# Kernel optimization log

Measured on AMD Instinct MI355X. Metric: run time of the kernel, lower is better.

Reference implementation:

```python
import jax, jax.numpy as jnp
import numpy as np

DIM = 1024
NUM_HEADS = 16
DIM_HEAD = 64
FEATURE_DIM = 64
INNER = NUM_HEADS * DIM_HEAD
EPS = 1e-6


def setup_inputs() -> dict:
    key = jax.random.key(0)
    ks = jax.random.split(key, 7)
    x = jax.random.normal(ks[0], (4, 8192, DIM), dtype=jnp.float32)
    s = 1.0 / np.sqrt(DIM)
    Wq = jax.random.normal(ks[1], (DIM, INNER), dtype=jnp.float32) * s
    Wk = jax.random.normal(ks[2], (DIM, INNER), dtype=jnp.float32) * s
    Wv = jax.random.normal(ks[3], (DIM, INNER), dtype=jnp.float32) * s
    proj = jax.random.normal(ks[4], (DIM_HEAD, FEATURE_DIM), dtype=jnp.float32) / np.sqrt(FEATURE_DIM)
    Wo = jax.random.normal(ks[5], (INNER, DIM), dtype=jnp.float32) * (1.0 / np.sqrt(INNER))
    bo = jnp.zeros((DIM,), dtype=jnp.float32)
    return {"x": x, "Wq": Wq, "Wk": Wk, "Wv": Wv, "proj": proj, "Wo": Wo, "bo": bo}


def _feature_map(t, proj):
    # t: [b, h, n, d] -> relu(t @ proj) + eps : [b, h, n, f]
    return jax.nn.relu(jnp.einsum('bhnd,df->bhnf', t, proj)) + EPS


def reference(x, Wq, Wk, Wv, proj, Wo, bo):
    b, n, _ = x.shape
    def split_heads(t):
        return t.reshape(b, n, NUM_HEADS, DIM_HEAD).transpose(0, 2, 1, 3)  # [b,h,n,d]
    q = split_heads(x @ Wq)
    k = split_heads(x @ Wk)
    v = split_heads(x @ Wv)
    qf = _feature_map(q, proj)  # [b,h,n,f]
    kf = _feature_map(k, proj)  # [b,h,n,f]
    kv = jnp.einsum('bhnf,bhnd->bhfd', kf, v)          # [b,h,f,d]
    k_sum = kf.sum(axis=-2)                             # [b,h,f]
    num = jnp.einsum('bhnf,bhfd->bhnd', qf, kv)         # [b,h,n,d]
    den = jnp.einsum('bhnf,bhf->bhn', qf, k_sum) + EPS  # [b,h,n]
    out = num / den[..., None]
    out = out.transpose(0, 2, 1, 3).reshape(b, n, INNER)
    return out @ Wo + bo
```

## Files before the change

kernel.cpp:

```cpp
#include <hip/hip_runtime.h>

typedef unsigned short u16;
typedef unsigned int u32;
typedef __attribute__((ext_vector_type(4))) float f32x4;
typedef __attribute__((ext_vector_type(4))) u16 u16x4;
typedef __attribute__((ext_vector_type(8))) u16 u16x8;
typedef __attribute__((ext_vector_type(8))) __bf16 bf16x8;

#define FLA_EPS 1e-6f

__device__ __forceinline__ u16 f2b(float f) {
  union { float f; u32 u; } v; v.f = f;
  u32 r = v.u + 0x7FFFu + ((v.u >> 16) & 1u);
  return (u16)(r >> 16);
}
__device__ __forceinline__ float b2f(u16 h) {
  union { u32 u; float f; } v; v.u = ((u32)h) << 16; return v.f;
}
__device__ __forceinline__ void g2l16(const void* g, void* l) {
  __builtin_amdgcn_global_load_lds((__attribute__((address_space(1))) void*)g,
                                   (__attribute__((address_space(3))) void*)l,
                                   16, 0, 0);
}

__global__ void __launch_bounds__(256) cast_f32_bf16(const float* __restrict__ in,
                                                     u16* __restrict__ out) {
  size_t i = (size_t)blockIdx.x * 256 + threadIdx.x;
  const f32x4* p = (const f32x4*)in + i * 2;
  f32x4 a = p[0], b = p[1];
  u16x8 r;
  r[0] = f2b(a[0]); r[1] = f2b(a[1]); r[2] = f2b(a[2]); r[3] = f2b(a[3]);
  r[4] = f2b(b[0]); r[5] = f2b(b[1]); r[6] = f2b(b[2]); r[7] = f2b(b[3]);
  ((u16x8*)out)[i] = r;
}

__global__ void __launch_bounds__(256) transpose_cast(const float* __restrict__ W,
                                                      u16* __restrict__ Wt, int dim) {
  __shared__ float tile[64][65];
  const int t = threadIdx.x;
  const int k0 = blockIdx.x * 64, n0 = blockIdx.y * 64;
  const int r = t >> 4, c4 = (t & 15) * 4;
#pragma unroll
  for (int i = 0; i < 4; ++i) {
    f32x4 vv = *(const f32x4*)(W + (size_t)(k0 + r + i * 16) * dim + n0 + c4);
    tile[r + i * 16][c4 + 0] = vv[0];
    tile[r + i * 16][c4 + 1] = vv[1];
    tile[r + i * 16][c4 + 2] = vv[2];
    tile[r + i * 16][c4 + 3] = vv[3];
  }
  __syncthreads();
#pragma unroll
  for (int i = 0; i < 4; ++i) {
    int nrow = r + i * 16;
    u16x4 o;
#pragma unroll
    for (int j = 0; j < 4; ++j) o[j] = f2b(tile[c4 + j][nrow]);
    *(u16x4*)(Wt + (size_t)(n0 + nrow) * dim + k0 + c4) = o;
  }
}

__global__ void __launch_bounds__(256) fold_w(const float* __restrict__ Wq,
                                              const float* __restrict__ Wk,
                                              const float* __restrict__ proj,
                                              u16* __restrict__ WqkvT) {
  __shared__ float Wt[64][65];
  __shared__ float P[64][64];
  const int t = threadIdx.x;
  const int kbase = blockIdx.x * 64, h = blockIdx.y, sel = blockIdx.z;
  const float* W = sel ? Wk : Wq;
  {
    int row = t >> 2, cb = (t & 3) * 16;
#pragma unroll
    for (int i = 0; i < 4; ++i) {
      f32x4 vv = *(const f32x4*)(W + (size_t)(kbase + row) * 1024 + h * 64 + cb + i * 4);
      Wt[row][cb + i * 4 + 0] = vv[0]; Wt[row][cb + i * 4 + 1] = vv[1];
      Wt[row][cb + i * 4 + 2] = vv[2]; Wt[row][cb + i * 4 + 3] = vv[3];
      f32x4 pp = *(const f32x4*)(proj + (size_t)row * 64 + cb + i * 4);
      P[row][cb + i * 4 + 0] = pp[0]; P[row][cb + i * 4 + 1] = pp[1];
      P[row][cb + i * 4 + 2] = pp[2]; P[row][cb + i * 4 + 3] = pp[3];
    }
  }
  __syncthreads();
  const int kk = t & 63, fg = (t >> 6) * 16;
  float acc[16] = {};
  for (int d = 0; d < 64; ++d) {
    float w = Wt[kk][d];
#pragma unroll
    for (int ff = 0; ff < 16; ++ff) acc[ff] = fmaf(w, P[d][fg + ff], acc[ff]);
  }
#pragma unroll
  for (int ff = 0; ff < 16; ++ff)
    WqkvT[(size_t)(sel * 1024 + h * 64 + fg + ff) * 1024 + kbase + kk] = f2b(acc[ff]);
}

template <int NB, bool QKV>
__global__ void __launch_bounds__(512, 2) gemm256(const u16* __restrict__ Ax,
                                                  const u16* __restrict__ Bt,
                                                  u16* __restrict__ qo, u16* __restrict__ ko,
                                                  u16* __restrict__ vo,
                                                  float* __restrict__ Cf,
                                                  const float* __restrict__ bias) {
  extern __shared__ __align__(16) u16 lds[];
  const int tid = threadIdx.x;
  const int flat = blockIdx.x;
  const int xcd = flat & 7, slot = flat >> 3;
  const int pos = slot & 7, g = slot >> 3;
  const int nc = g % NB, mc = g / NB;
  const int m0 = (xcd * 16 + mc * 8 + pos) * 256;
  const int n0 = nc * 256;
  const int w = tid >> 6, l = tid & 63, quad = l >> 4, lr = l & 15;
  const int wm = w >> 2, wn = w & 3;
  u16* const A0 = lds;
  u16* const B0 = lds + 16384;
  u16* const A1 = lds + 32768;
  u16* const B1 = lds + 49152;
  const int c0 = ((quad * 16) ^ ((lr & 7) << 4)) >> 1;
  const int c1 = ((64 + quad * 16) ^ ((lr & 7) << 4)) >> 1;
  const int rst = tid >> 3;
  const int ksw8 = ((tid & 7) ^ (rst & 7)) * 8;
  const int tid8 = tid * 8;

  f32x4 acc[8][4] = {};
  bf16x8 af[4][2], bf[4][2];

#define STG(SRC, ROW0, KT, DST) do {                                         \
    const u16* s_ = (SRC) + (size_t)((ROW0) + rst) * 1024 + (KT) + ksw8;     \
    g2l16(s_, (DST) + tid8);                                                 \
    g2l16(s_ + 64 * 1024, (DST) + 4096 + tid8);                              \
  } while (0)

#define LDA_(BASE, MH) do {                                                  \
    const u16* ap_ = (BASE) + wm * 8192;                                     \
    _Pragma("unroll")                                                        \
    for (int ii = 0; ii < 4; ++ii) {                                         \
      const int ro_ = ((MH) * 64 + ii * 16 + lr) * 64;                       \
      af[ii][0] = *(const bf16x8*)(ap_ + ro_ + c0);                          \
      af[ii][1] = *(const bf16x8*)(ap_ + ro_ + c1);                          \
    } } while (0)

#define LDB_(BASE, NH) do {                                                  \
    const u16* bp_ = (BASE) + (wn >> 1) * 8192 + (wn & 1) * 4096;            \
    _Pragma("unroll")                                                        \
    for (int jj = 0; jj < 2; ++jj) {                                         \
      const int ro_ = (((NH) * 2 + jj) * 16 + lr) * 64;                      \
      bf[(NH) * 2 + jj][0] = *(const bf16x8*)(bp_ + ro_ + c0);               \
      bf[(NH) * 2 + jj][1] = *(const bf16x8*)(bp_ + ro_ + c1);               \
    } } while (0)

#define MFMA16(MH, NH)                                                       \
    _Pragma("unroll")                                                        \
    for (int ii = 0; ii < 4; ++ii)                                           \
      _Pragma("unroll")                                                      \
      for (int jj = 0; jj < 2; ++jj)                                         \
        _Pragma("unroll")                                                    \
        for (int ks = 0; ks < 2; ++ks)                                       \
          acc[(MH) * 4 + ii][(NH) * 2 + jj] =                                \
              __builtin_amdgcn_mfma_f32_16x16x32_bf16(                       \
                  af[ii][ks], bf[(NH) * 2 + jj][ks],                         \
                  acc[(MH) * 4 + ii][(NH) * 2 + jj], 0, 0, 0);

#define BARMFMA(MH, NH) do {                                                 \
    __builtin_amdgcn_s_barrier();                                            \
    asm volatile("s_waitcnt lgkmcnt(0)" ::: "memory");                       \
    __builtin_amdgcn_sched_barrier(0);                                       \
    __builtin_amdgcn_s_setprio(1);                                           \
    MFMA16(MH, NH);                                                          \
    __builtin_amdgcn_s_setprio(0);                                           \
    __builtin_amdgcn_s_barrier();                                            \
  } while (0)

  STG(Ax, m0, 0, A0);  STG(Ax, m0 + 128, 0, A0 + 8192);
  STG(Bt, n0, 0, B0);  STG(Bt, n0 + 128, 0, B0 + 8192);
  STG(Bt, n0, 64, B1); STG(Bt, n0 + 128, 64, B1 + 8192);
  asm volatile("s_waitcnt vmcnt(4)" ::: "memory");
  __builtin_amdgcn_s_barrier();

  for (int it = 0; it < 8; ++it) {
    const bool lastI = (it == 7);
    const int ko = it * 128;
    LDA_(A0, 0); LDB_(B0, 0);
    STG(Ax, m0, ko + 64, A1);
    BARMFMA(0, 0);
    LDB_(B0, 1);
    STG(Ax, m0 + 128, ko + 64, A1 + 8192);
    BARMFMA(0, 1);
    LDA_(A0, 1);
    if (!lastI) STG(Bt, n0, ko + 128, B0);
    BARMFMA(1, 0);
    if (!lastI) {
      STG(Bt, n0 + 128, ko + 128, B0 + 8192);
      asm volatile("s_waitcnt vmcnt(4)" ::: "memory");
    } else {
      asm volatile("s_waitcnt vmcnt(0)" ::: "memory");
    }
    BARMFMA(1, 1);
    LDA_(A1, 0); LDB_(B1, 0);
    if (!lastI) STG(Ax, m0, ko + 128, A0);
    BARMFMA(0, 0);
    LDB_(B1, 1);
    if (!lastI) STG(Ax, m0 + 128, ko + 128, A0 + 8192);
    BARMFMA(0, 1);
    LDA_(A1, 1);
    if (!lastI) STG(Bt, n0, ko + 192, B1);
    BARMFMA(1, 0);
    if (!lastI) {
      STG(Bt, n0 + 128, ko + 192, B1 + 8192);
      asm volatile("s_waitcnt vmcnt(4)" ::: "memory");
    }
    BARMFMA(1, 1);
  }
#undef STG
#undef LDA_
#undef LDB_
#undef MFMA16
#undef BARMFMA

  const int rbase = m0 + wm * 128 + quad * 4;
  if (QKV) {
    const int sel = n0 >> 10;
    u16* dst = (sel == 0) ? qo : ((sel == 1) ? ko : vo);
    const int cb = (n0 & 1023) + wn * 64 + lr;
#pragma unroll
    for (int mi = 0; mi < 8; ++mi)
#pragma unroll
      for (int nj = 0; nj < 4; ++nj)
#pragma unroll
        for (int rr = 0; rr < 4; ++rr) {
          int row = rbase + mi * 16 + rr;
          float v = acc[mi][nj][rr];
          if (sel < 2) v = fmaxf(v, 0.0f) + FLA_EPS;
          dst[(size_t)row * 1024 + cb + nj * 16] = f2b(v);
        }
  } else {
    const int cb = n0 + wn * 64 + lr;
#pragma unroll
    for (int mi = 0; mi < 8; ++mi)
#pragma unroll
      for (int nj = 0; nj < 4; ++nj)
#pragma unroll
        for (int rr = 0; rr < 4; ++rr) {
          int row = rbase + mi * 16 + rr;
          Cf[(size_t)row * 1024 + cb + nj * 16] = acc[mi][nj][rr] + bias[cb + nj * 16];
        }
  }
}

__global__ void __launch_bounds__(256) kv_partial(const u16* __restrict__ kf,
                                                  const u16* __restrict__ v,
                                                  float* __restrict__ part,
                                                  float* __restrict__ ksum_p) {
  const int t = threadIdx.x;
  const int bh = blockIdx.x, b = bh >> 4, h = bh & 15;
  const int w = t >> 6, l = t & 63;
  const int sub = blockIdx.y * 4 + w;
  const int f0 = (l >> 3) * 8, d0 = (l & 7) * 8;
  const size_t rowbase = ((size_t)b * 8192 + (size_t)sub * 256) * 1024 + h * 64;
  float acc[8][8] = {};
  float ks[8] = {};
#pragma unroll 2
  for (int n = 0; n < 256; ++n) {
    u16x8 ka = *(const u16x8*)(kf + rowbase + (size_t)n * 1024 + f0);
    u16x8 va = *(const u16x8*)(v + rowbase + (size_t)n * 1024 + d0);
    float kff[8], vf[8];
#pragma unroll
    for (int i = 0; i < 8; ++i) { kff[i] = b2f(ka[i]); vf[i] = b2f(va[i]); }
#pragma unroll
    for (int i = 0; i < 8; ++i) {
      ks[i] += kff[i];
#pragma unroll
      for (int j = 0; j < 8; ++j) acc[i][j] = fmaf(kff[i], vf[j], acc[i][j]);
    }
  }
  float* pb = part + ((size_t)bh * 32 + sub) * 4096;
#pragma unroll
  for (int j = 0; j < 8; ++j)
#pragma unroll
    for (int i = 0; i < 8; i += 4) {
      f32x4 vv = { acc[i][j], acc[i + 1][j], acc[i + 2][j], acc[i + 3][j] };
      *(f32x4*)(pb + (d0 + j) * 64 + f0 + i) = vv;
    }
  if (d0 == 0) {
    float* kp = ksum_p + ((size_t)bh * 32 + sub) * 64 + f0;
    f32x4 a = { ks[0], ks[1], ks[2], ks[3] }, bq = { ks[4], ks[5], ks[6], ks[7] };
    *(f32x4*)(kp) = a; *(f32x4*)(kp + 4) = bq;
  }
}

__global__ void __launch_bounds__(256) reduce_kv(const float* __restrict__ part,
                                                 float* __restrict__ kvT) {
  int i = blockIdx.x * 256 + threadIdx.x;
  int bh = i >> 12, dfi = i & 4095;
  const float* p = part + (size_t)bh * 32 * 4096 + dfi;
  float s = 0.f;
#pragma unroll
  for (int sub = 0; sub < 32; ++sub) s += p[(size_t)sub * 4096];
  kvT[i] = s;
}

__global__ void __launch_bounds__(256) num_den(const u16* __restrict__ qf,
                                               const float* __restrict__ kvT,
                                               const float* __restrict__ ksum_p,
                                               u16* __restrict__ outI) {
  __shared__ __align__(16) u16 As[128 * 64];
  __shared__ __align__(16) u16 Bs[64 * 64];
  __shared__ float ksum_s[64];
  __shared__ float den_s[128];
  const int t = threadIdx.x;
  const size_t tok0 = (size_t)blockIdx.x * 128;
  const int h = blockIdx.y;
  const int bh = (blockIdx.x >> 6) * 16 + h;
  const int w = t >> 6, l = t & 63, quad = l >> 4, lr = l & 15;
  const int trow = t >> 3, tcol = (t & 7) * 8;
#pragma unroll
  for (int i = 0; i < 4; ++i) {
    int r = i * 32 + trow;
    g2l16(qf + (tok0 + r) * 1024 + h * 64 + tcol, &As[r * 64 + tcol]);
  }
  {
    const float* kvb = kvT + (size_t)bh * 4096;
    int d = t >> 2, cb = (t & 3) * 16;
    u16x8 o0, o1;
#pragma unroll
    for (int q4 = 0; q4 < 2; ++q4) {
      f32x4 vv = *(const f32x4*)(kvb + d * 64 + cb + q4 * 4);
      o0[q4 * 4 + 0] = f2b(vv[0]); o0[q4 * 4 + 1] = f2b(vv[1]);
      o0[q4 * 4 + 2] = f2b(vv[2]); o0[q4 * 4 + 3] = f2b(vv[3]);
    }
#pragma unroll
    for (int q4 = 0; q4 < 2; ++q4) {
      f32x4 vv = *(const f32x4*)(kvb + d * 64 + cb + 8 + q4 * 4);
      o1[q4 * 4 + 0] = f2b(vv[0]); o1[q4 * 4 + 1] = f2b(vv[1]);
      o1[q4 * 4 + 2] = f2b(vv[2]); o1[q4 * 4 + 3] = f2b(vv[3]);
    }
    *(u16x8*)&Bs[d * 64 + cb] = o0;
    *(u16x8*)&Bs[d * 64 + cb + 8] = o1;
  }
  if (t < 64) {
    float s = 0.f;
    const float* kp = ksum_p + (size_t)bh * 32 * 64 + t;
#pragma unroll
    for (int sub = 0; sub < 32; ++sub) s += kp[(size_t)sub * 64];
    ksum_s[t] = s;
  }
  __syncthreads();
  if (t < 128) {
    float d = FLA_EPS;
#pragma unroll
    for (int jj = 0; jj < 64; ++jj) {
      int f = (t + jj) & 63;
      d += b2f(As[t * 64 + f]) * ksum_s[f];
    }
    den_s[t] = d;
  }
  __syncthreads();
  f32x4 acc[2][4] = {};
  const int wrow = w * 32;
#pragma unroll
  for (int ks = 0; ks < 2; ++ks) {
    bf16x8 af[2], bfr[4];
#pragma unroll
    for (int i = 0; i < 2; ++i)
      af[i] = *(const bf16x8*)&As[(wrow + i * 16 + lr) * 64 + ks * 32 + quad * 8];
#pragma unroll
    for (int j = 0; j < 4; ++j)
      bfr[j] = *(const bf16x8*)&Bs[(j * 16 + lr) * 64 + ks * 32 + quad * 8];
#pragma unroll
    for (int i = 0; i < 2; ++i)
#pragma unroll
      for (int j = 0; j < 4; ++j)
        acc[i][j] = __builtin_amdgcn_mfma_f32_16x16x32_bf16(af[i], bfr[j], acc[i][j], 0, 0, 0);
  }
#pragma unroll
  for (int i = 0; i < 2; ++i)
#pragma unroll
    for (int j = 0; j < 4; ++j)
#pragma unroll
      for (int rr = 0; rr < 4; ++rr) {
        int rloc = wrow + i * 16 + quad * 4 + rr;
        float v = acc[i][j][rr] / den_s[rloc];
        outI[(tok0 + rloc) * 1024 + h * 64 + j * 16 + lr] = f2b(v);
      }
}

extern "C" void kernel_launch(void* const* d_in, const int* in_sizes, int n_in,
                              void* d_out, int out_size, void* d_ws, size_t ws_size,
                              hipStream_t stream) {
  const float* x    = (const float*)d_in[0];
  const float* Wq   = (const float*)d_in[1];
  const float* Wk   = (const float*)d_in[2];
  const float* Wv   = (const float*)d_in[3];
  const float* proj = (const float*)d_in[4];
  const float* Wo   = (const float*)d_in[5];
  const float* bo   = (const float*)d_in[6];
  float* out = (float*)d_out;

  char* ws = (char*)d_ws;
  const size_t SZ = 1ull << 26;
  u16* xb     = (u16*)(ws + 0);
  u16* qb     = (u16*)(ws + SZ);
  u16* kb     = (u16*)(ws + 2 * SZ);
  u16* vb     = (u16*)(ws + 3 * SZ);
  u16* WqkvT  = (u16*)(ws + 4 * SZ);
  u16* woT    = (u16*)(ws + 4 * SZ + 0x600000);
  float* part   = (float*)(ws + 4 * SZ + 0x800000);
  float* ksum_p = (float*)(ws + 4 * SZ + 0x800000 + 0x2000000);
  float* kvT    = (float*)(ws + 4 * SZ + 0x800000 + 0x2080000);

  static int attr_done = 0;
  if (!attr_done) {
    (void)hipFuncSetAttribute((const void*)gemm256<12, true>,
                              hipFuncAttributeMaxDynamicSharedMemorySize, 131072);
    (void)hipFuncSetAttribute((const void*)gemm256<4, false>,
                              hipFuncAttributeMaxDynamicSharedMemorySize, 131072);
    attr_done = 1;
  }

  cast_f32_bf16<<<16384, 256, 0, stream>>>(x, xb);
  fold_w<<<dim3(16, 16, 2), 256, 0, stream>>>(Wq, Wk, proj, WqkvT);
  transpose_cast<<<dim3(16, 16), 256, 0, stream>>>(Wv, WqkvT + (size_t)2048 * 1024, 1024);
  transpose_cast<<<dim3(16, 16), 256, 0, stream>>>(Wo, woT, 1024);
  gemm256<12, true><<<1536, 512, 131072, stream>>>(xb, WqkvT, qb, kb, vb, nullptr, nullptr);
  kv_partial<<<dim3(64, 8), 256, 0, stream>>>(kb, vb, part, ksum_p);
  reduce_kv<<<1024, 256, 0, stream>>>(part, kvT);
  num_den<<<dim3(256, 16), 256, 0, stream>>>(qb, kvT, ksum_p, xb);
  gemm256<4, false><<<512, 512, 131072, stream>>>(xb, woT, nullptr, nullptr, nullptr, out, bo);
}
```

Baseline: 657.0 us.

## Restructure GEMM main loop with register double-buffered LDS fragments and fewer barriers

Rewrites the GEMM K-loop as a per-64-slice TILE step. A and B fragments are double-buffered in registers (af0/af1, bfA/bfB), so the LDS reads for the next cluster are issued while the current MFMA cluster runs, gated by partial lgkmcnt waits rather than full drains. It removes the barrier pair around every MFMA cluster, leaving about two barriers per K-slice, and changes the global-to-LDS staging order to prefetch A and B further ahead. The cost is more fragment registers, which may lower occupancy or cause spills, and fragile hand-tuned waitcnt ordering that could race if a count is wrong.

```diff
diff --git a/kernel.cpp b/kernel.cpp
--- a/kernel.cpp
+++ b/kernel.cpp
@@ -121,7 +121,7 @@
   const int tid8 = tid * 8;
 
   f32x4 acc[8][4] = {};
-  bf16x8 af[4][2], bf[4][2];
+  bf16x8 af0[4][2], af1[4][2], bfA[4][2], bfB[4][2];
 
 #define STG(SRC, ROW0, KT, DST) do {                                         \
     const u16* s_ = (SRC) + (size_t)((ROW0) + rst) * 1024 + (KT) + ksw8;     \
@@ -129,25 +129,26 @@
     g2l16(s_ + 64 * 1024, (DST) + 4096 + tid8);                              \
   } while (0)
 
-#define LDA_(BASE, MH) do {                                                  \
-    const u16* ap_ = (BASE) + wm * 8192;                                     \
+#define RD_A(DSTA, BASE, MH) do {                                            \
+    const u16* ap_ = (BASE) + wm * 8192 + (MH) * 4096;                       \
     _Pragma("unroll")                                                        \
     for (int ii = 0; ii < 4; ++ii) {                                         \
-      const int ro_ = ((MH) * 64 + ii * 16 + lr) * 64;                       \
-      af[ii][0] = *(const bf16x8*)(ap_ + ro_ + c0);                          \
-      af[ii][1] = *(const bf16x8*)(ap_ + ro_ + c1);                          \
+      const int ro_ = (ii * 16 + lr) * 64;                                   \
+      DSTA[ii][0] = *(const bf16x8*)(ap_ + ro_ + c0);                        \
+      DSTA[ii][1] = *(const bf16x8*)(ap_ + ro_ + c1);                        \
     } } while (0)
 
-#define LDB_(BASE, NH) do {                                                  \
+#define RD_B(DSTB, BASE) do {                                                \
     const u16* bp_ = (BASE) + (wn >> 1) * 8192 + (wn & 1) * 4096;            \
     _Pragma("unroll")                                                        \
-    for (int jj = 0; jj < 2; ++jj) {                                         \
-      const int ro_ = (((NH) * 2 + jj) * 16 + lr) * 64;                      \
-      bf[(NH) * 2 + jj][0] = *(const bf16x8*)(bp_ + ro_ + c0);               \
-      bf[(NH) * 2 + jj][1] = *(const bf16x8*)(bp_ + ro_ + c1);               \
+    for (int jj = 0; jj < 4; ++jj) {                                         \
+      const int ro_ = (jj * 16 + lr) * 64;                                   \
+      DSTB[jj][0] = *(const bf16x8*)(bp_ + ro_ + c0);                        \
+      DSTB[jj][1] = *(const bf16x8*)(bp_ + ro_ + c1);                        \
     } } while (0)
 
-#define MFMA16(MH, NH)                                                       \
+#define CLUSTER(AF, MH, BFS, NH) do {                                        \
+    __builtin_amdgcn_s_setprio(1);                                           \
     _Pragma("unroll")                                                        \
     for (int ii = 0; ii < 4; ++ii)                                           \
       _Pragma("unroll")                                                      \
@@ -156,64 +157,70 @@
         for (int ks = 0; ks < 2; ++ks)                                       \
           acc[(MH) * 4 + ii][(NH) * 2 + jj] =                                \
               __builtin_amdgcn_mfma_f32_16x16x32_bf16(                       \
-                  af[ii][ks], bf[(NH) * 2 + jj][ks],                         \
-                  acc[(MH) * 4 + ii][(NH) * 2 + jj], 0, 0, 0);
-
-#define BARMFMA(MH, NH) do {                                                 \
-    __builtin_amdgcn_s_barrier();                                            \
-    asm volatile("s_waitcnt lgkmcnt(0)" ::: "memory");                       \
-    __builtin_amdgcn_sched_barrier(0);                                       \
-    __builtin_amdgcn_s_setprio(1);                                           \
-    MFMA16(MH, NH);                                                          \
+                  AF[ii][ks], BFS[(NH) * 2 + jj][ks],                        \
+                  acc[(MH) * 4 + ii][(NH) * 2 + jj], 0, 0, 0);               \
     __builtin_amdgcn_s_setprio(0);                                           \
-    __builtin_amdgcn_s_barrier();                                            \
   } while (0)
 
-  STG(Ax, m0, 0, A0);  STG(Ax, m0 + 128, 0, A0 + 8192);
-  STG(Bt, n0, 0, B0);  STG(Bt, n0 + 128, 0, B0 + 8192);
+#define WAIT_LGKM8() do { asm volatile("s_waitcnt lgkmcnt(8)" ::: "memory"); \
+    __builtin_amdgcn_sched_barrier(0); } while (0)
+#define WAIT_LGKM0() do { asm volatile("s_waitcnt lgkmcnt(0)" ::: "memory"); \
+    __builtin_amdgcn_sched_barrier(0); } while (0)
+#define WAIT_VM0()  do { asm volatile("s_waitcnt vmcnt(0)" ::: "memory");    \
+    __builtin_amdgcn_sched_barrier(0); } while (0)
+#define BARRIER()   do { asm volatile("s_barrier" ::: "memory"); } while (0)
+
+#define TILE(TV, ABUF, BBUF, ABUFN, BBUFN, BFC, BFN) do {                    \
+    const int t_ = (TV);                                                     \
+    if (t_ > 0 && t_ < 15) {                                                 \
+      STG(Ax, m0, (t_ + 1) * 64, ABUFN);                                     \
+      STG(Ax, m0 + 128, (t_ + 1) * 64, (ABUFN) + 8192);                      \
+    }                                                                        \
+    RD_A(af1, ABUF, 1);                                                      \
+    WAIT_LGKM8();                                                            \
+    CLUSTER(af0, 0, BFC, 0);                                                 \
+    CLUSTER(af0, 0, BFC, 1);                                                 \
+    if (t_ < 15) {                                                           \
+      WAIT_VM0();                                                            \
+      BARRIER();                                                             \
+      if (t_ < 14) {                                                         \
+        STG(Bt, n0, (t_ + 2) * 64, BBUF);                                    \
+        STG(Bt, n0 + 128, (t_ + 2) * 64, (BBUF) + 8192);                     \
+      }                                                                      \
+      RD_B(BFN, BBUFN);                                                      \
+      WAIT_LGKM8();                                                          \
+    } else {                                                                 \
+      WAIT_LGKM0();                                                          \
+    }                                                                        \
+    CLUSTER(af1, 1, BFC, 0);                                                 \
+    if (t_ < 15) RD_A(af0, ABUFN, 0);                                        \
+    CLUSTER(af1, 1, BFC, 1);                                                 \
+    if (t_ < 15) BARRIER();                                                  \
+  } while (0)
+
+  STG(Ax, m0, 0, A0); STG(Ax, m0 + 128, 0, A0 + 8192);
+  STG(Bt, n0, 0, B0); STG(Bt, n0 + 128, 0, B0 + 8192);
+  STG(Ax, m0, 64, A1); STG(Ax, m0 + 128, 64, A1 + 8192);
   STG(Bt, n0, 64, B1); STG(Bt, n0 + 128, 64, B1 + 8192);
-  asm volatile("s_waitcnt vmcnt(4)" ::: "memory");
-  __builtin_amdgcn_s_barrier();
+  asm volatile("s_waitcnt vmcnt(8)" ::: "memory");
+  __builtin_amdgcn_sched_barrier(0);
+  BARRIER();
+  RD_B(bfA, B0);
+  RD_A(af0, A0, 0);
 
   for (int it = 0; it < 8; ++it) {
-    const bool lastI = (it == 7);
-    const int ko = it * 128;
-    LDA_(A0, 0); LDB_(B0, 0);
-    STG(Ax, m0, ko + 64, A1);
-    BARMFMA(0, 0);
-    LDB_(B0, 1);
-    STG(Ax, m0 + 128, ko + 64, A1 + 8192);
-    BARMFMA(0, 1);
-    LDA_(A0, 1);
-    if (!lastI) STG(Bt, n0, ko + 128, B0);
-    BARMFMA(1, 0);
-    if (!lastI) {
-      STG(Bt, n0 + 128, ko + 128, B0 + 8192);
-      asm volatile("s_waitcnt vmcnt(4)" ::: "memory");
-    } else {
-      asm volatile("s_waitcnt vmcnt(0)" ::: "memory");
-    }
-    BARMFMA(1, 1);
-    LDA_(A1, 0); LDB_(B1, 0);
-    if (!lastI) STG(Ax, m0, ko + 128, A0);
-    BARMFMA(0, 0);
-    LDB_(B1, 1);
-    if (!lastI) STG(Ax, m0 + 128, ko + 128, A0 + 8192);
-    BARMFMA(0, 1);
-    LDA_(A1, 1);
-    if (!lastI) STG(Bt, n0, ko + 192, B1);
-    BARMFMA(1, 0);
-    if (!lastI) {
-      STG(Bt, n0 + 128, ko + 192, B1 + 8192);
-      asm volatile("s_waitcnt vmcnt(4)" ::: "memory");
-    }
-    BARMFMA(1, 1);
-  }
+    TILE(2 * it,     A0, B0, A1, B1, bfA, bfB);
+    TILE(2 * it + 1, A1, B1, A0, B0, bfB, bfA);
+  }
+#undef TILE
 #undef STG
-#undef LDA_
-#undef LDB_
-#undef MFMA16
-#undef BARMFMA
+#undef RD_A
+#undef RD_B
+#undef CLUSTER
+#undef WAIT_LGKM8
+#undef WAIT_LGKM0
+#undef WAIT_VM0
+#undef BARRIER
 
   const int rbase = m0 + wm * 128 + quad * 4;
   if (QKV) {
```

Result: slower. 894.2 us (+36.1%).
